# Performance work log

Hardware: AMD Instinct MI355X
Metric: run time of the kernel (lower is better)

## Reference

```python
import jax, jax.numpy as jnp
import numpy as np

E, H, D = 512, 8, 64
B, T = 2, 1024
HD = H * D


def _linear(x, W, b):
    return x @ W + b


def _ln(x, g, b):
    mu = x.mean(-1, keepdims=True)
    var = ((x - mu) ** 2).mean(-1, keepdims=True)
    return (x - mu) / jnp.sqrt(var + 1e-5) * g + b


def _l2norm(x):
    n = jnp.sqrt((x * x).sum(-1, keepdims=True))
    return x / jnp.maximum(n, 1e-12)


def setup_inputs() -> dict:
    key = jax.random.key(0)
    ks = jax.random.split(key, 32)
    s = 0.02
    inp = {
        'x': jax.random.normal(ks[0], (B, T, E), jnp.float32),
        'b_min': jax.random.normal(ks[1], (B, T, E), jnp.float32),
        'b_max': jax.random.normal(ks[2], (B, T, E), jnp.float32),
        'motif_context': jax.random.normal(ks[3], (B, T, E), jnp.float32),
        'Wk': jax.random.normal(ks[4], (E, HD), jnp.float32) * s,
        'bk': jnp.zeros((HD,), jnp.float32),
        'Wq': jax.random.normal(ks[5], (E, HD), jnp.float32) * s,
        'bq': jnp.zeros((HD,), jnp.float32),
        'Wv': jax.random.normal(ks[6], (E, HD), jnp.float32) * s,
        'bv': jnp.zeros((HD,), jnp.float32),
        'Wo': jax.random.normal(ks[7], (HD, E), jnp.float32) * s,
        'bo': jnp.zeros((E,), jnp.float32),
        'Wd': jax.random.normal(ks[8], (E, H), jnp.float32) * s,
        'bd': jnp.zeros((H,), jnp.float32),
        'Wgw': jax.random.normal(ks[9], (E, H), jnp.float32) * s,
        'bgw': jnp.zeros((H,), jnp.float32),
        'Wgf': jax.random.normal(ks[10], (E, H), jnp.float32) * s,
        'bgf': jnp.zeros((H,), jnp.float32),
        'Wps': jax.random.normal(ks[11], (E, E), jnp.float32) * s,
        'bps': jnp.zeros((E,), jnp.float32),
        'ln1_g': jnp.ones((E,), jnp.float32),
        'ln1_b': jnp.zeros((E,), jnp.float32),
        'ln2_g': jnp.ones((E,), jnp.float32),
        'ln2_b': jnp.zeros((E,), jnp.float32),
        'W1': jax.random.normal(ks[12], (E, 4 * E), jnp.float32) * s,
        'b1': jnp.zeros((4 * E,), jnp.float32),
        'W2': jax.random.normal(ks[13], (4 * E, E), jnp.float32) * s,
        'b2': jnp.zeros((E,), jnp.float32),
    }
    return inp


def reference(x, b_min, b_max, motif_context,
              Wk, bk, Wq, bq, Wv, bv, Wo, bo, Wd, bd,
              Wgw, bgw, Wgf, bgf, Wps, bps,
              ln1_g, ln1_b, ln2_g, ln2_b, W1, b1, W2, b2):
    Bs, Ts, Es = x.shape
    x_n = _ln(x, ln1_g, ln1_b)
    k = _l2norm(_linear(x_n, Wk, bk).reshape(Bs, Ts, H, D))
    q = _l2norm(_linear(x_n, Wq, bq).reshape(Bs, Ts, H, D))
    v = jnp.tanh(_linear(x_n, Wv, bv).reshape(Bs, Ts, H, D))
    d = jax.nn.softplus(_linear(x_n, Wd, bd))            # (B,T,H)
    gw = jax.nn.sigmoid(_linear(x_n, Wgw, bgw)) ** 2     # (B,T,H)
    gf = 1.0 - jax.nn.sigmoid(_linear(x_n, Wgf, bgf)) ** 2

    # gated linear recurrent scan via cumsum of rank-1 updates
    v_gated = v * (d * gw)[..., None]                    # (B,T,H,D)
    updates = jnp.einsum('bthi,bthj->bthij', v_gated, k)  # (B,T,H,D,D)
    decay = jnp.clip(d * gf, 1e-6, 0.999)
    log_decay = jnp.log(decay)[..., None, None]          # (B,T,H,1,1)
    exp_cum_decay = jnp.exp(jnp.cumsum(log_decay, axis=1))
    state = jnp.cumsum(updates / (exp_cum_decay + 1e-8), axis=1) * exp_cum_decay
    readout = jnp.einsum('bthij,bthj->bthi', state, q)   # (B,T,H,D)
    next_mem = state[:, -1]

    x2 = x + _linear(readout.reshape(Bs, Ts, HD), Wo, bo) + 0.1 * motif_context
    h = _ln(x2, ln2_g, ln2_b)
    x3 = x2 + _linear(jax.nn.gelu(_linear(h, W1, b1), approximate=False), W2, b2)
    probe = _linear(x3, Wps, bps)
    return (x3, next_mem, b_min + probe, b_max + probe)
```

## Files before the change

kernel.cpp:

```cpp
#include <hip/hip_runtime.h>


typedef unsigned short u16;
typedef unsigned int u32;
typedef __attribute__((ext_vector_type(8))) short short8;
typedef __attribute__((ext_vector_type(4))) float floatx4;

__device__ __forceinline__ float b2f(u16 u) {
  u32 x = ((u32)u) << 16;
  return __uint_as_float(x);
}
__device__ __forceinline__ u16 f2b(float f) {
  u32 x = __float_as_uint(f);
  u32 r = (x + 0x7fffu + ((x >> 16) & 1u)) >> 16;
  return (u16)r;
}
__device__ __forceinline__ float4 b4_to_f4(uint2 u) {
  float4 r;
  r.x = __uint_as_float((u.x & 0xffffu) << 16);
  r.y = __uint_as_float(u.x & 0xffff0000u);
  r.z = __uint_as_float((u.y & 0xffffu) << 16);
  r.w = __uint_as_float(u.y & 0xffff0000u);
  return r;
}

__device__ __forceinline__ void stage16(const u16* g, u16* lds_wave_base) {
  __builtin_amdgcn_global_load_lds((const __attribute__((address_space(1))) void*)g,
                                   (__attribute__((address_space(3))) void*)lds_wave_base,
                                   16, 0, 0);
}

template <int ROWS>
__device__ __forceinline__ void stage_tile64(const u16* __restrict__ G, int ldK, int kb,
                                             u16* lds, int tid) {
#pragma unroll
  for (int r = 0; r < ROWS / 32; ++r) {
    int slot = r * 256 + tid;
    int row = slot >> 3;
    int kwg = (slot & 7) ^ (row & 7);
    stage16(G + (size_t)row * ldK + kb * 64 + kwg * 8,
            lds + (size_t)(r * 256 + (tid >> 6) * 64) * 8);
  }
}

__device__ __forceinline__ void ln_row(const float* __restrict__ xr,
                                       const float* __restrict__ g,
                                       const float* __restrict__ bt,
                                       u16* __restrict__ yr, int tid, float* red) {
  float x0 = xr[tid], x1 = xr[tid + 256];
  float s = x0 + x1, ss = x0 * x0 + x1 * x1;
#pragma unroll
  for (int o = 32; o > 0; o >>= 1) { s += __shfl_xor(s, o); ss += __shfl_xor(ss, o); }
  if ((tid & 63) == 0) { red[tid >> 6] = s; red[4 + (tid >> 6)] = ss; }
  __syncthreads();
  float ts = red[0] + red[1] + red[2] + red[3];
  float tss = red[4] + red[5] + red[6] + red[7];
  float mu = ts * (1.f / 512.f);
  float var = tss * (1.f / 512.f) - mu * mu;
  float rstd = 1.0f / sqrtf(var + 1e-5f);
  yr[tid] = f2b((x0 - mu) * rstd * g[tid] + bt[tid]);
  yr[tid + 256] = f2b((x1 - mu) * rstd * g[tid + 256] + bt[tid + 256]);
}

__global__ __launch_bounds__(256) void prep_weights(
    const float* __restrict__ Wk, const float* __restrict__ Wq,
    const float* __restrict__ Wv, const float* __restrict__ Wo,
    const float* __restrict__ Wps, const float* __restrict__ W1,
    const float* __restrict__ W2, const float* __restrict__ Wd,
    const float* __restrict__ Wgw, const float* __restrict__ Wgf,
    const float* __restrict__ bk, const float* __restrict__ bq,
    const float* __restrict__ bv, const float* __restrict__ bd,
    const float* __restrict__ bgw, const float* __restrict__ bgf,
    const float* __restrict__ x, const float* __restrict__ ln1g,
    const float* __restrict__ ln1b,
    u16* __restrict__ WTQ, u16* __restrict__ WTO, u16* __restrict__ WTPS,
    u16* __restrict__ WT1, u16* __restrict__ WT2, float* __restrict__ BQV,
    u16* __restrict__ XN) {
  int bid = blockIdx.x, tid = threadIdx.x;
  __shared__ float tile[32][33];
  __shared__ float red[8];
  if (bid < 3328) {
    const float* src;
    u16* dst;
    int C, rel, tiles_x;
    if (bid < 256)       { src = Wk;  dst = WTQ;           C = 512;  rel = bid;        tiles_x = 16; }
    else if (bid < 512)  { src = Wq;  dst = WTQ + 262144;  C = 512;  rel = bid - 256;  tiles_x = 16; }
    else if (bid < 768)  { src = Wv;  dst = WTQ + 524288;  C = 512;  rel = bid - 512;  tiles_x = 16; }
    else if (bid < 1024) { src = Wo;  dst = WTO;           C = 512;  rel = bid - 768;  tiles_x = 16; }
    else if (bid < 1280) { src = Wps; dst = WTPS;          C = 512;  rel = bid - 1024; tiles_x = 16; }
    else if (bid < 2304) { src = W1;  dst = WT1;           C = 2048; rel = bid - 1280; tiles_x = 64; }
    else                 { src = W2;  dst = WT2;           C = 512;  rel = bid - 2304; tiles_x = 16; }
    int R = (bid >= 1280 && bid < 2304) ? 512 : (bid >= 2304 ? 2048 : 512);
    int c0 = (rel % tiles_x) * 32, r0 = (rel / tiles_x) * 32;
    int tx = tid & 31, ty = tid >> 5;
#pragma unroll
    for (int i = 0; i < 4; ++i)
      tile[ty + i * 8][tx] = src[(size_t)(r0 + ty + i * 8) * C + c0 + tx];
    __syncthreads();
#pragma unroll
    for (int i = 0; i < 4; ++i)
      dst[(size_t)(c0 + ty + i * 8) * R + r0 + tx] = f2b(tile[tx][ty + i * 8]);
  } else if (bid < 3392) {
    int idx = (bid - 3328) * 256 + tid;
    const int stride = 64 * 256;
    for (int i = idx; i < 128 * 512; i += stride) {
      int local = i >> 9, k = i & 511;
      float v = 0.f;
      if (local < 8) v = Wd[k * 8 + local];
      else if (local < 16) v = Wgw[k * 8 + (local - 8)];
      else if (local < 24) v = Wgf[k * 8 + (local - 16)];
      WTQ[(size_t)(1536 + local) * 512 + k] = f2b(v);
    }
    for (int i = idx; i < 1664; i += stride) {
      float v = 0.f;
      if (i < 512) v = bk[i];
      else if (i < 1024) v = bq[i - 512];
      else if (i < 1536) v = bv[i - 1024];
      else if (i < 1544) v = bd[i - 1536];
      else if (i < 1552) v = bgw[i - 1544];
      else if (i < 1560) v = bgf[i - 1552];
      BQV[i] = v;
    }
  } else {
    int row = bid - 3392;
    ln_row(x + (size_t)row * 512, ln1g, ln1b, XN + (size_t)row * 512, tid, red);
  }
}

__global__ __launch_bounds__(256) void ln_f32(const float* __restrict__ X,
                                              const float* __restrict__ g,
                                              const float* __restrict__ bt,
                                              u16* __restrict__ Y) {
  __shared__ float red[8];
  ln_row(X + (size_t)blockIdx.x * 512, g, bt, Y + (size_t)blockIdx.x * 512,
         threadIdx.x, red);
}

template <int BM, int EPI>
__global__ __launch_bounds__(256, (BM == 64 ? 3 : 4)) void gemm64k(
    const u16* __restrict__ A, const u16* __restrict__ BT, const float* __restrict__ bias,
    float* __restrict__ outf, float* __restrict__ outf2, u16* __restrict__ outb,
    const float* __restrict__ aux0, const float* __restrict__ aux1, int M, int N, int K) {
  constexpr int MT = BM / 32;
  constexpr int S = BM / 32 + 2;
  __shared__ __align__(16) u16 As[3][BM * 64];
  __shared__ __align__(16) u16 Bs[3][64 * 64];
  const int tid = threadIdx.x;
  const int lane = tid & 63, wave = tid >> 6;
  const int wm = wave >> 1, wn = wave & 1;
  const int m0 = blockIdx.y * BM, n0 = blockIdx.x * 64;
  floatx4 acc[MT][2] = {};
  const int fr = lane & 15, kq = lane >> 4;
  const int nk = K >> 6;
  const u16* Ab = A + (size_t)m0 * K;
  const u16* Bb = BT + (size_t)n0 * K;

  stage_tile64<BM>(Ab, K, 0, As[0], tid);
  stage_tile64<64>(Bb, K, 0, Bs[0], tid);
  if (nk > 1) {
    stage_tile64<BM>(Ab, K, 1, As[1], tid);
    stage_tile64<64>(Bb, K, 1, Bs[1], tid);
  }

  for (int kb = 0; kb < nk; ++kb) {
    const int cur = kb % 3;
    if (kb + 2 < nk) {
      const int nxt = (kb + 2) % 3;
      stage_tile64<BM>(Ab, K, kb + 2, As[nxt], tid);
      stage_tile64<64>(Bb, K, kb + 2, Bs[nxt], tid);
    }
    int ahead = nk - 1 - kb;
    if (ahead > 2) ahead = 2;
    if (ahead == 2) {
      if constexpr (S == 4) asm volatile("s_waitcnt vmcnt(8)" ::: "memory");
      else asm volatile("s_waitcnt vmcnt(6)" ::: "memory");
    } else if (ahead == 1) {
      if constexpr (S == 4) asm volatile("s_waitcnt vmcnt(4)" ::: "memory");
      else asm volatile("s_waitcnt vmcnt(3)" ::: "memory");
    } else {
      asm volatile("s_waitcnt vmcnt(0)" ::: "memory");
    }
    asm volatile("s_barrier" ::: "memory");

#pragma unroll
    for (int sub = 0; sub < 2; ++sub) {
      short8 af[MT], bf[2];
#pragma unroll
      for (int mt = 0; mt < MT; ++mt) {
        int row = wm * (BM / 2) + mt * 16 + fr;
        int c = sub * 4 + kq;
        af[mt] = *(const short8*)&As[cur][row * 64 + ((c ^ (row & 7)) << 3)];
      }
#pragma unroll
      for (int nt = 0; nt < 2; ++nt) {
        int row = wn * 32 + nt * 16 + fr;
        int c = sub * 4 + kq;
        bf[nt] = *(const short8*)&Bs[cur][row * 64 + ((c ^ (row & 7)) << 3)];
      }
#pragma unroll
      for (int mt = 0; mt < MT; ++mt)
#pragma unroll
        for (int nt = 0; nt < 2; ++nt)
          acc[mt][nt] =
              __builtin_amdgcn_mfma_f32_16x16x32_bf16(af[mt], bf[nt], acc[mt][nt], 0, 0, 0);
    }
    asm volatile("s_waitcnt lgkmcnt(0)" ::: "memory");
    asm volatile("s_barrier" ::: "memory");
  }

  const int col = lane & 15;
  const int rbase = (lane >> 4) * 4;
#pragma unroll
  for (int nt = 0; nt < 2; ++nt) {
    int gc = n0 + wn * 32 + nt * 16 + col;
    float bvv = bias[gc];
#pragma unroll
    for (int mt = 0; mt < MT; ++mt) {
      int gr = m0 + wm * (BM / 2) + mt * 16 + rbase;
#pragma unroll
      for (int r = 0; r < 4; ++r) {
        size_t idx = (size_t)(gr + r) * N + gc;
        float v = acc[mt][nt][r] + bvv;
        if constexpr (EPI == 0) {
          outf[idx] = v;
        } else if constexpr (EPI == 1) {
          outf[idx] = aux0[idx] + v + 0.1f * aux1[idx];
        } else if constexpr (EPI == 2) {
          outb[idx] = f2b(0.5f * v * (1.f + erff(v * 0.70710678118654752f)));
        } else if constexpr (EPI == 3) {
          float w = aux0[idx] + v;
          outf[idx] = w;
          outb[idx] = f2b(w);
        } else {
          outf[idx] = aux0[idx] + v;
          outf2[idx] = aux1[idx] + v;
        }
      }
    }
  }
}

__global__ __launch_bounds__(512) void post_qkvg(const float* __restrict__ C0,
                                                 u16* __restrict__ KB, u16* __restrict__ QB,
                                                 u16* __restrict__ VG,
                                                 float* __restrict__ DEC) {
  int tok = blockIdx.x;
  int b = tok >> 10, t = tok & 1023;
  int tid = threadIdx.x;
  int h = tid >> 6, d = tid & 63;
  const float* row = C0 + (size_t)tok * 1664;

  float dl = row[1536 + h], gwl = row[1544 + h], gfl = row[1552 + h];
  float dd = dl > 20.f ? dl : log1pf(expf(dl));
  float sw = 1.f / (1.f + expf(-gwl));
  float gw = sw * sw;
  float sf = 1.f / (1.f + expf(-gfl));
  float gf = 1.f - sf * sf;

  size_t obase = ((size_t)(b * 8 + h) * 1024 + t) * 64 + d;

  float kx = row[h * 64 + d];
  float ssk = kx * kx;
#pragma unroll
  for (int o = 32; o > 0; o >>= 1) ssk += __shfl_xor(ssk, o);
  KB[obase] = f2b(kx / fmaxf(sqrtf(ssk), 1e-12f));

  float qx = row[512 + h * 64 + d];
  float ssq = qx * qx;
#pragma unroll
  for (int o = 32; o > 0; o >>= 1) ssq += __shfl_xor(ssq, o);
  QB[obase] = f2b(qx / fmaxf(sqrtf(ssq), 1e-12f));

  float vx = tanhf(row[1024 + h * 64 + d]);
  VG[obase] = f2b(vx * (dd * gw));

  if (d == 0)
    DEC[(size_t)(b * 8 + h) * 1024 + t] = fminf(fmaxf(dd * gf, 1e-6f), 0.999f);
}

__global__ void logcum(const float* __restrict__ DEC, float* __restrict__ LC,
                       float* __restrict__ WW) {
  int bh = blockIdx.x;
  int lane = threadIdx.x;
  size_t base = (size_t)bh * 1024 + lane * 16;
  float loc[16];
  float run = 0.f;
#pragma unroll
  for (int i = 0; i < 16; ++i) { run += logf(DEC[base + i]); loc[i] = run; }
  float x = run;
#pragma unroll
  for (int o = 1; o < 64; o <<= 1) {
    float v = __shfl_up(x, o);
    if (lane >= o) x += v;
  }
  float excl = x - run;
#pragma unroll
  for (int i = 0; i < 16; ++i) {
    float L = excl + loc[i];
    LC[base + i] = L;
    float c = expf(L);
    WW[base + i] = c / (c + 1e-8f);
  }
}

__global__ __launch_bounds__(256, 2) void scan_phase1(
    const u16* __restrict__ KB, const u16* __restrict__ QB, const u16* __restrict__ VG,
    const float* __restrict__ DEC, const float* __restrict__ WW,
    float* __restrict__ RP, float* __restrict__ SF) {
  int chunk = blockIdx.x, h = blockIdx.y, b = blockIdx.z;
  int bh = b * 8 + h;
  int t0 = chunk * 64;
  __shared__ __align__(16) float sk[4096], sq[4096], sv[4096];
  __shared__ float lsa[64], lsw[64];
  int tid = threadIdx.x, lane = tid & 63, wave = tid >> 6;

  const u16* gk = KB + ((size_t)bh * 1024 + t0) * 64;
  const u16* gq = QB + ((size_t)bh * 1024 + t0) * 64;
  const u16* gv = VG + ((size_t)bh * 1024 + t0) * 64;
#pragma unroll
  for (int r = 0; r < 4; ++r) {
    int f = ((wave * 4 + r) * 64 + lane) * 4;
    *(float4*)&sk[f] = b4_to_f4(*(const uint2*)(gk + f));
    *(float4*)&sq[f] = b4_to_f4(*(const uint2*)(gq + f));
    *(float4*)&sv[f] = b4_to_f4(*(const uint2*)(gv + f));
  }
  if (tid < 64) {
    lsa[tid] = DEC[(size_t)bh * 1024 + t0 + tid];
    lsw[tid] = WW[(size_t)bh * 1024 + t0 + tid];
  }
  __syncthreads();

  int i = tid >> 2, j0 = (tid & 3) * 16;
  float s[16];
#pragma unroll
  for (int z = 0; z < 16; ++z) s[z] = 0.f;

  for (int t = 0; t < 64; ++t) {
    float a = lsa[t], w = lsw[t];
    float wv = w * sv[t * 64 + i];
    float r = 0.f;
#pragma unroll
    for (int u4 = 0; u4 < 4; ++u4) {
      float4 kv = *(const float4*)&sk[t * 64 + j0 + u4 * 4];
      float4 qv = *(const float4*)&sq[t * 64 + j0 + u4 * 4];
      s[u4 * 4 + 0] = fmaf(a, s[u4 * 4 + 0], wv * kv.x); r = fmaf(s[u4 * 4 + 0], qv.x, r);
      s[u4 * 4 + 1] = fmaf(a, s[u4 * 4 + 1], wv * kv.y); r = fmaf(s[u4 * 4 + 1], qv.y, r);
      s[u4 * 4 + 2] = fmaf(a, s[u4 * 4 + 2], wv * kv.z); r = fmaf(s[u4 * 4 + 2], qv.z, r);
      s[u4 * 4 + 3] = fmaf(a, s[u4 * 4 + 3], wv * kv.w); r = fmaf(s[u4 * 4 + 3], qv.w, r);
    }
    r += __shfl_xor(r, 1);
    r += __shfl_xor(r, 2);
    if ((tid & 3) == 0)
      RP[((size_t)(b * 1024 + t0 + t) * 8 + h) * 64 + i] = r;
  }

  float* Sf = SF + ((size_t)bh * 16 + chunk) * 4096 + i * 64 + j0;
#pragma unroll
  for (int u4 = 0; u4 < 4; ++u4) {
    float4 v;
    v.x = s[u4 * 4 + 0]; v.y = s[u4 * 4 + 1]; v.z = s[u4 * 4 + 2]; v.w = s[u4 * 4 + 3];
    *(float4*)&Sf[u4 * 4] = v;
  }
}

__global__ __launch_bounds__(256) void scan_phase2p(const float* __restrict__ SF,
                                                    const float* __restrict__ LC,
                                                    float* __restrict__ SI,
                                                    float* __restrict__ next_mem) {
  int bh = blockIdx.x >> 4;
  int e = (blockIdx.x & 15) * 256 + threadIdx.x;
  float s = 0.f;
  for (int c = 0; c < 16; ++c) {
    SI[((size_t)bh * 16 + c) * 4096 + e] = s;
    float Lend = LC[(size_t)bh * 1024 + c * 64 + 63];
    float Lpre = c ? LC[(size_t)bh * 1024 + c * 64 - 1] : 0.f;
    float P = expf(Lend - Lpre);
    s = fmaf(P, s, SF[((size_t)bh * 16 + c) * 4096 + e]);
  }
  next_mem[(size_t)bh * 4096 + e] = s;
}

__global__ __launch_bounds__(256, 2) void scan_phase3(
    const u16* __restrict__ QB, const float* __restrict__ SI, const float* __restrict__ LC,
    const float* __restrict__ RP, u16* __restrict__ AB) {
  int chunk = blockIdx.x, h = blockIdx.y, b = blockIdx.z;
  int bh = b * 8 + h;
  int t0 = chunk * 64;
  __shared__ __align__(16) float sq[4096];
  __shared__ float sL[64];
  int tid = threadIdx.x, lane = tid & 63, wave = tid >> 6;

  const u16* gq = QB + ((size_t)bh * 1024 + t0) * 64;
#pragma unroll
  for (int r = 0; r < 4; ++r) {
    int f = ((wave * 4 + r) * 64 + lane) * 4;
    *(float4*)&sq[f] = b4_to_f4(*(const uint2*)(gq + f));
  }
  if (tid < 64) sL[tid] = LC[(size_t)bh * 1024 + t0 + tid];
  __syncthreads();

  float Lpre = chunk ? LC[(size_t)bh * 1024 + t0 - 1] : 0.f;
  int i = tid >> 2, j0 = (tid & 3) * 16;
  const float* Si = SI + ((size_t)bh * 16 + chunk) * 4096 + i * 64 + j0;
  float S[16];
#pragma unroll
  for (int u4 = 0; u4 < 4; ++u4) {
    float4 v = *(const float4*)&Si[u4 * 4];
    S[u4 * 4 + 0] = v.x; S[u4 * 4 + 1] = v.y; S[u4 * 4 + 2] = v.z; S[u4 * 4 + 3] = v.w;
  }

  for (int t = 0; t < 64; ++t) {
    float p = expf(sL[t] - Lpre);
    float r = 0.f;
#pragma unroll
    for (int u4 = 0; u4 < 4; ++u4) {
      float4 qv = *(const float4*)&sq[t * 64 + j0 + u4 * 4];
      r = fmaf(S[u4 * 4 + 0], qv.x, r);
      r = fmaf(S[u4 * 4 + 1], qv.y, r);
      r = fmaf(S[u4 * 4 + 2], qv.z, r);
      r = fmaf(S[u4 * 4 + 3], qv.w, r);
    }
    r += __shfl_xor(r, 1);
    r += __shfl_xor(r, 2);
    if ((tid & 3) == 0) {
      size_t gi = ((size_t)(b * 1024 + t0 + t) * 8 + h) * 64 + i;
      AB[gi] = f2b(RP[gi] + p * r);
    }
  }
}

extern "C" void kernel_launch(void* const* d_in, const int* in_sizes, int n_in,
                              void* d_out, int out_size, void* d_ws, size_t ws_size,
                              hipStream_t stream) {
  const float* x = (const float*)d_in[0];
  const float* bmin = (const float*)d_in[1];
  const float* bmax = (const float*)d_in[2];
  const float* motif = (const float*)d_in[3];
  const float* Wk = (const float*)d_in[4];
  const float* bk = (const float*)d_in[5];
  const float* Wq = (const float*)d_in[6];
  const float* bq = (const float*)d_in[7];
  const float* Wv = (const float*)d_in[8];
  const float* bv = (const float*)d_in[9];
  const float* Wo = (const float*)d_in[10];
  const float* bo = (const float*)d_in[11];
  const float* Wd = (const float*)d_in[12];
  const float* bd = (const float*)d_in[13];
  const float* Wgw = (const float*)d_in[14];
  const float* bgw = (const float*)d_in[15];
  const float* Wgf = (const float*)d_in[16];
  const float* bgf = (const float*)d_in[17];
  const float* Wps = (const float*)d_in[18];
  const float* bps = (const float*)d_in[19];
  const float* ln1g = (const float*)d_in[20];
  const float* ln1b = (const float*)d_in[21];
  const float* ln2g = (const float*)d_in[22];
  const float* ln2b = (const float*)d_in[23];
  const float* W1 = (const float*)d_in[24];
  const float* b1 = (const float*)d_in[25];
  const float* W2 = (const float*)d_in[26];
  const float* b2 = (const float*)d_in[27];

  char* ws = (char*)d_ws;
  u16* WTQ = (u16*)(ws + 0);
  u16* WTO = (u16*)(ws + 1703936);
  u16* WT1 = (u16*)(ws + 2228224);
  u16* WT2 = (u16*)(ws + 4325376);
  u16* WTPS = (u16*)(ws + 6422528);
  float* BQV = (float*)(ws + 6946816);
  u16* XN = (u16*)(ws + 6953984);
  float* C0 = (float*)(ws + 9051136);
  u16* KB = (u16*)(ws + 25828352);
  u16* QB = (u16*)(ws + 27925504);
  u16* VG = (u16*)(ws + 30022656);
  float* DEC = (float*)(ws + 32119808);
  float* LC = (float*)(ws + 32185344);
  float* WW = (float*)(ws + 32250880);
  float* RP = (float*)(ws + 32316416);
  float* SF = (float*)(ws + 36510720);
  float* SI = (float*)(ws + 40705024);
  u16* AB = (u16*)(ws + 9051136);
  float* X2 = (float*)(ws + 11148288);
  u16* HB = (u16*)(ws + 15342592);
  u16* MID = (u16*)(ws + 17439744);
  u16* X3B = (u16*)(ws + 25828352);

  float* out0 = (float*)d_out;
  float* out1 = out0 + 1048576;
  float* out2 = out0 + 1114112;
  float* out3 = out0 + 2162688;

  prep_weights<<<5440, 256, 0, stream>>>(Wk, Wq, Wv, Wo, Wps, W1, W2, Wd, Wgw, Wgf,
                                         bk, bq, bv, bd, bgw, bgf, x, ln1g, ln1b,
                                         WTQ, WTO, WTPS, WT1, WT2, BQV, XN);
  gemm64k<64, 0><<<dim3(26, 32), 256, 0, stream>>>(XN, WTQ, BQV, C0, nullptr, nullptr,
                                                   nullptr, nullptr, 2048, 1664, 512);
  post_qkvg<<<2048, 512, 0, stream>>>(C0, KB, QB, VG, DEC);
  logcum<<<16, 64, 0, stream>>>(DEC, LC, WW);
  scan_phase1<<<dim3(16, 8, 2), 256, 0, stream>>>(KB, QB, VG, DEC, WW, RP, SF);
  scan_phase2p<<<256, 256, 0, stream>>>(SF, LC, SI, out1);
  scan_phase3<<<dim3(16, 8, 2), 256, 0, stream>>>(QB, SI, LC, RP, AB);

  gemm64k<32, 1><<<dim3(8, 64), 256, 0, stream>>>(AB, WTO, bo, X2, nullptr, nullptr,
                                                  x, motif, 2048, 512, 512);
  ln_f32<<<2048, 256, 0, stream>>>(X2, ln2g, ln2b, HB);
  gemm64k<64, 2><<<dim3(32, 32), 256, 0, stream>>>(HB, WT1, b1, nullptr, nullptr, MID,
                                                   nullptr, nullptr, 2048, 2048, 512);
  gemm64k<32, 3><<<dim3(8, 64), 256, 0, stream>>>(MID, WT2, b2, out0, nullptr, X3B,
                                                  X2, nullptr, 2048, 512, 2048);
  gemm64k<32, 4><<<dim3(8, 64), 256, 0, stream>>>(X3B, WTPS, bps, out2, out3, nullptr,
                                                  bmin, bmax, 2048, 512, 512);
}
```

Baseline: 258.7 us.

## Switch GEMMs to double-buffered LDS and halve scan chunk length

The GEMM kernel moves from a three-stage LDS ring to a two-stage double buffer and raises the occupancy hint in launch_bounds, trading prefetch depth for more resident blocks. The chunked linear-recurrence scan uses 32-step chunks instead of 64, doubling the grid of phase1/phase3 to 512 blocks. This gives more parallelism but doubles the per-chunk state buffers and the sequential length of phase2. Workspace offsets are repacked to fit the larger SF/SI buffers.

```diff
diff --git a/kernel.cpp b/kernel.cpp
--- a/kernel.cpp
+++ b/kernel.cpp
@@ -137,14 +137,14 @@
 }
 
 template <int BM, int EPI>
-__global__ __launch_bounds__(256, (BM == 64 ? 3 : 4)) void gemm64k(
+__global__ __launch_bounds__(256, (BM == 64 ? 4 : 6)) void gemm2s(
     const u16* __restrict__ A, const u16* __restrict__ BT, const float* __restrict__ bias,
     float* __restrict__ outf, float* __restrict__ outf2, u16* __restrict__ outb,
     const float* __restrict__ aux0, const float* __restrict__ aux1, int M, int N, int K) {
   constexpr int MT = BM / 32;
   constexpr int S = BM / 32 + 2;
-  __shared__ __align__(16) u16 As[3][BM * 64];
-  __shared__ __align__(16) u16 Bs[3][64 * 64];
+  __shared__ __align__(16) u16 As[2][BM * 64];
+  __shared__ __align__(16) u16 Bs[2][64 * 64];
   const int tid = threadIdx.x;
   const int lane = tid & 63, wave = tid >> 6;
   const int wm = wave >> 1, wn = wave & 1;
@@ -157,24 +157,12 @@
 
   stage_tile64<BM>(Ab, K, 0, As[0], tid);
   stage_tile64<64>(Bb, K, 0, Bs[0], tid);
-  if (nk > 1) {
-    stage_tile64<BM>(Ab, K, 1, As[1], tid);
-    stage_tile64<64>(Bb, K, 1, Bs[1], tid);
-  }
 
   for (int kb = 0; kb < nk; ++kb) {
-    const int cur = kb % 3;
-    if (kb + 2 < nk) {
-      const int nxt = (kb + 2) % 3;
-      stage_tile64<BM>(Ab, K, kb + 2, As[nxt], tid);
-      stage_tile64<64>(Bb, K, kb + 2, Bs[nxt], tid);
-    }
-    int ahead = nk - 1 - kb;
-    if (ahead > 2) ahead = 2;
-    if (ahead == 2) {
-      if constexpr (S == 4) asm volatile("s_waitcnt vmcnt(8)" ::: "memory");
-      else asm volatile("s_waitcnt vmcnt(6)" ::: "memory");
-    } else if (ahead == 1) {
+    const int cur = kb & 1;
+    if (kb + 1 < nk) {
+      stage_tile64<BM>(Ab, K, kb + 1, As[cur ^ 1], tid);
+      stage_tile64<64>(Bb, K, kb + 1, Bs[cur ^ 1], tid);
       if constexpr (S == 4) asm volatile("s_waitcnt vmcnt(4)" ::: "memory");
       else asm volatile("s_waitcnt vmcnt(3)" ::: "memory");
     } else {
@@ -309,22 +297,22 @@
     float* __restrict__ RP, float* __restrict__ SF) {
   int chunk = blockIdx.x, h = blockIdx.y, b = blockIdx.z;
   int bh = b * 8 + h;
-  int t0 = chunk * 64;
-  __shared__ __align__(16) float sk[4096], sq[4096], sv[4096];
-  __shared__ float lsa[64], lsw[64];
-  int tid = threadIdx.x, lane = tid & 63, wave = tid >> 6;
+  int t0 = chunk * 32;
+  __shared__ __align__(16) float sk[2048], sq[2048], sv[2048];
+  __shared__ float lsa[32], lsw[32];
+  int tid = threadIdx.x;
 
   const u16* gk = KB + ((size_t)bh * 1024 + t0) * 64;
   const u16* gq = QB + ((size_t)bh * 1024 + t0) * 64;
   const u16* gv = VG + ((size_t)bh * 1024 + t0) * 64;
 #pragma unroll
-  for (int r = 0; r < 4; ++r) {
-    int f = ((wave * 4 + r) * 64 + lane) * 4;
+  for (int r = 0; r < 2; ++r) {
+    int f = (r * 256 + tid) * 4;
     *(float4*)&sk[f] = b4_to_f4(*(const uint2*)(gk + f));
     *(float4*)&sq[f] = b4_to_f4(*(const uint2*)(gq + f));
     *(float4*)&sv[f] = b4_to_f4(*(const uint2*)(gv + f));
   }
-  if (tid < 64) {
+  if (tid < 32) {
     lsa[tid] = DEC[(size_t)bh * 1024 + t0 + tid];
     lsw[tid] = WW[(size_t)bh * 1024 + t0 + tid];
   }
@@ -335,7 +323,7 @@
 #pragma unroll
   for (int z = 0; z < 16; ++z) s[z] = 0.f;
 
-  for (int t = 0; t < 64; ++t) {
+  for (int t = 0; t < 32; ++t) {
     float a = lsa[t], w = lsw[t];
     float wv = w * sv[t * 64 + i];
     float r = 0.f;
@@ -354,7 +342,7 @@
       RP[((size_t)(b * 1024 + t0 + t) * 8 + h) * 64 + i] = r;
   }
 
-  float* Sf = SF + ((size_t)bh * 16 + chunk) * 4096 + i * 64 + j0;
+  float* Sf = SF + ((size_t)bh * 32 + chunk) * 4096 + i * 64 + j0;
 #pragma unroll
   for (int u4 = 0; u4 < 4; ++u4) {
     float4 v;
@@ -370,12 +358,12 @@
   int bh = blockIdx.x >> 4;
   int e = (blockIdx.x & 15) * 256 + threadIdx.x;
   float s = 0.f;
-  for (int c = 0; c < 16; ++c) {
-    SI[((size_t)bh * 16 + c) * 4096 + e] = s;
-    float Lend = LC[(size_t)bh * 1024 + c * 64 + 63];
-    float Lpre = c ? LC[(size_t)bh * 1024 + c * 64 - 1] : 0.f;
+  for (int c = 0; c < 32; ++c) {
+    SI[((size_t)bh * 32 + c) * 4096 + e] = s;
+    float Lend = LC[(size_t)bh * 1024 + c * 32 + 31];
+    float Lpre = c ? LC[(size_t)bh * 1024 + c * 32 - 1] : 0.f;
     float P = expf(Lend - Lpre);
-    s = fmaf(P, s, SF[((size_t)bh * 16 + c) * 4096 + e]);
+    s = fmaf(P, s, SF[((size_t)bh * 32 + c) * 4096 + e]);
   }
   next_mem[(size_t)bh * 4096 + e] = s;
 }
@@ -385,23 +373,23 @@
     const float* __restrict__ RP, u16* __restrict__ AB) {
   int chunk = blockIdx.x, h = blockIdx.y, b = blockIdx.z;
   int bh = b * 8 + h;
-  int t0 = chunk * 64;
-  __shared__ __align__(16) float sq[4096];
-  __shared__ float sL[64];
-  int tid = threadIdx.x, lane = tid & 63, wave = tid >> 6;
+  int t0 = chunk * 32;
+  __shared__ __align__(16) float sq[2048];
+  __shared__ float sL[32];
+  int tid = threadIdx.x;
 
   const u16* gq = QB + ((size_t)bh * 1024 + t0) * 64;
 #pragma unroll
-  for (int r = 0; r < 4; ++r) {
-    int f = ((wave * 4 + r) * 64 + lane) * 4;
+  for (int r = 0; r < 2; ++r) {
+    int f = (r * 256 + tid) * 4;
     *(float4*)&sq[f] = b4_to_f4(*(const uint2*)(gq + f));
   }
-  if (tid < 64) sL[tid] = LC[(size_t)bh * 1024 + t0 + tid];
+  if (tid < 32) sL[tid] = LC[(size_t)bh * 1024 + t0 + tid];
   __syncthreads();
 
   float Lpre = chunk ? LC[(size_t)bh * 1024 + t0 - 1] : 0.f;
   int i = tid >> 2, j0 = (tid & 3) * 16;
-  const float* Si = SI + ((size_t)bh * 16 + chunk) * 4096 + i * 64 + j0;
+  const float* Si = SI + ((size_t)bh * 32 + chunk) * 4096 + i * 64 + j0;
   float S[16];
 #pragma unroll
   for (int u4 = 0; u4 < 4; ++u4) {
@@ -409,7 +397,7 @@
     S[u4 * 4 + 0] = v.x; S[u4 * 4 + 1] = v.y; S[u4 * 4 + 2] = v.z; S[u4 * 4 + 3] = v.w;
   }
 
-  for (int t = 0; t < 64; ++t) {
+  for (int t = 0; t < 32; ++t) {
     float p = expf(sL[t] - Lpre);
     float r = 0.f;
 #pragma unroll
@@ -470,20 +458,20 @@
   float* BQV = (float*)(ws + 6946816);
   u16* XN = (u16*)(ws + 6953984);
   float* C0 = (float*)(ws + 9051136);
-  u16* KB = (u16*)(ws + 25828352);
-  u16* QB = (u16*)(ws + 27925504);
-  u16* VG = (u16*)(ws + 30022656);
-  float* DEC = (float*)(ws + 32119808);
-  float* LC = (float*)(ws + 32185344);
-  float* WW = (float*)(ws + 32250880);
-  float* RP = (float*)(ws + 32316416);
-  float* SF = (float*)(ws + 36510720);
-  float* SI = (float*)(ws + 40705024);
+  u16* KB = (u16*)(ws + 22682624);
+  u16* QB = (u16*)(ws + 24779776);
+  u16* VG = (u16*)(ws + 26876928);
+  float* DEC = (float*)(ws + 28974080);
+  float* LC = (float*)(ws + 29039616);
+  float* WW = (float*)(ws + 29105152);
+  float* RP = (float*)(ws + 29170688);
+  float* SF = (float*)(ws + 33364992);
+  float* SI = (float*)(ws + 41753600);
   u16* AB = (u16*)(ws + 9051136);
   float* X2 = (float*)(ws + 11148288);
   u16* HB = (u16*)(ws + 15342592);
   u16* MID = (u16*)(ws + 17439744);
-  u16* X3B = (u16*)(ws + 25828352);
+  u16* X3B = (u16*)(ws + 26876928);
 
   float* out0 = (float*)d_out;
   float* out1 = out0 + 1048576;
@@ -493,21 +481,21 @@
   prep_weights<<<5440, 256, 0, stream>>>(Wk, Wq, Wv, Wo, Wps, W1, W2, Wd, Wgw, Wgf,
                                          bk, bq, bv, bd, bgw, bgf, x, ln1g, ln1b,
                                          WTQ, WTO, WTPS, WT1, WT2, BQV, XN);
-  gemm64k<64, 0><<<dim3(26, 32), 256, 0, stream>>>(XN, WTQ, BQV, C0, nullptr, nullptr,
-                                                   nullptr, nullptr, 2048, 1664, 512);
+  gemm2s<64, 0><<<dim3(26, 32), 256, 0, stream>>>(XN, WTQ, BQV, C0, nullptr, nullptr,
+                                                  nullptr, nullptr, 2048, 1664, 512);
   post_qkvg<<<2048, 512, 0, stream>>>(C0, KB, QB, VG, DEC);
   logcum<<<16, 64, 0, stream>>>(DEC, LC, WW);
-  scan_phase1<<<dim3(16, 8, 2), 256, 0, stream>>>(KB, QB, VG, DEC, WW, RP, SF);
+  scan_phase1<<<dim3(32, 8, 2), 256, 0, stream>>>(KB, QB, VG, DEC, WW, RP, SF);
   scan_phase2p<<<256, 256, 0, stream>>>(SF, LC, SI, out1);
-  scan_phase3<<<dim3(16, 8, 2), 256, 0, stream>>>(QB, SI, LC, RP, AB);
-
-  gemm64k<32, 1><<<dim3(8, 64), 256, 0, stream>>>(AB, WTO, bo, X2, nullptr, nullptr,
-                                                  x, motif, 2048, 512, 512);
+  scan_phase3<<<dim3(32, 8, 2), 256, 0, stream>>>(QB, SI, LC, RP, AB);
+
+  gemm2s<32, 1><<<dim3(8, 64), 256, 0, stream>>>(AB, WTO, bo, X2, nullptr, nullptr,
+                                                 x, motif, 2048, 512, 512);
   ln_f32<<<2048, 256, 0, stream>>>(X2, ln2g, ln2b, HB);
-  gemm64k<64, 2><<<dim3(32, 32), 256, 0, stream>>>(HB, WT1, b1, nullptr, nullptr, MID,
-                                                   nullptr, nullptr, 2048, 2048, 512);
-  gemm64k<32, 3><<<dim3(8, 64), 256, 0, stream>>>(MID, WT2, b2, out0, nullptr, X3B,
-                                                  X2, nullptr, 2048, 512, 2048);
-  gemm64k<32, 4><<<dim3(8, 64), 256, 0, stream>>>(X3B, WTPS, bps, out2, out3, nullptr,
-                                                  bmin, bmax, 2048, 512, 512);
-}
+  gemm2s<64, 2><<<dim3(32, 32), 256, 0, stream>>>(HB, WT1, b1, nullptr, nullptr, MID,
+                                                  nullptr, nullptr, 2048, 2048, 512);
+  gemm2s<32, 3><<<dim3(8, 64), 256, 0, stream>>>(MID, WT2, b2, out0, nullptr, X3B,
+                                                 X2, nullptr, 2048, 512, 2048);
+  gemm2s<32, 4><<<dim3(8, 64), 256, 0, stream>>>(X3B, WTPS, bps, out2, out3, nullptr,
+                                                 bmin, bmax, 2048, 512, 512);
+}
```

Measured after the change: 234.7 us. 9.3% less time.
